# Kernel optimization log

Measured on AMD Instinct MI355X. Metric: run time of the kernel, lower is better.

Reference implementation:

```python
import jax, jax.numpy as jnp
import numpy as np

B, N, NUM_CLASSES, M, K = 64, 900, 128, 64, 8
COST_CLASS = 1.0
COST_BBOX = 5.0
INF = jnp.float32(1e9)


def _lsa(cost):
    """Jonker-Volgenant shortest-augmenting-path linear sum assignment.
    cost: [M, N] with M <= N (rows = targets, cols = predictions).
    Returns assigned column (prediction index) per row (target), shape [M] int32.
    Equivalent pairing to scipy.optimize.linear_sum_assignment."""
    Mr, Nc = cost.shape
    # column 0 is a dummy column (1-indexed columns, as in the classic formulation)
    a = jnp.concatenate([jnp.zeros((Mr, 1), cost.dtype), cost], axis=1)

    def assign_row(carry, i1):
        u, v, p = carry  # u:[M+1] row potentials, v:[N+1] col potentials, p:[N+1] row assigned to col (0=free)
        p = p.at[0].set(i1)
        init = (u, v, p,
                jnp.full(Nc + 1, INF, cost.dtype),   # minv
                jnp.zeros(Nc + 1, bool),             # used
                jnp.zeros(Nc + 1, jnp.int32),        # way (parent col)
                jnp.int32(0))                        # j0

        def cond(st):
            return st[2][st[6]] != 0

        def body(st):
            u, v, p, minv, used, way, j0 = st
            used = used.at[j0].set(True)
            i0 = p[j0]
            cur = a[i0 - 1] - u[i0] - v              # reduced costs of row i0 over all cols
            better = (cur < minv) & (~used)
            minv = jnp.where(better, cur, minv)
            way = jnp.where(better, j0, way)
            masked = jnp.where(used, INF, minv)
            j1 = jnp.argmin(masked).astype(jnp.int32)
            delta = masked[j1]
            u = u.at[p].add(jnp.where(used, delta, jnp.float32(0.0)))
            v = v - jnp.where(used, delta, jnp.float32(0.0))
            minv = jnp.where(used, minv, minv - delta)
            return (u, v, p, minv, used, way, j1)

        u, v, p, minv, used, way, j0 = jax.lax.while_loop(cond, body, init)

        def bt_body(st):  # backtrack the augmenting path
            p_, jj = st
            j1 = way[jj]
            return p_.at[jj].set(p_[j1]), j1

        p, _ = jax.lax.while_loop(lambda st: st[1] != 0, bt_body, (p, j0))
        return (u, v, p), None

    u0 = jnp.zeros(Mr + 1, cost.dtype)
    v0 = jnp.zeros(Nc + 1, cost.dtype)
    p0 = jnp.zeros(Nc + 1, jnp.int32)
    (u, v, p), _ = jax.lax.scan(assign_row, (u0, v0, p0),
                                jnp.arange(1, Mr + 1, dtype=jnp.int32))
    rows = p[1:]                                     # [N]: 1-indexed target row per pred col, 0 = free
    res = jnp.zeros(Mr, jnp.int32)
    res = res.at[jnp.where(rows > 0, rows - 1, Mr)].set(
        jnp.arange(Nc, dtype=jnp.int32), mode='drop')
    return res


def setup_inputs() -> dict:
    key = jax.random.key(0)
    k1, k2, k3, k4 = jax.random.split(key, 4)
    return {
        'class_logits': jax.random.normal(k1, (B, N, NUM_CLASSES), jnp.float32),
        'corners': jax.random.normal(k2, (B, N, K, 3), jnp.float32),
        'tgt_labels': jax.random.randint(k3, (B, M), 0, NUM_CLASSES, jnp.int32),
        'boxes': jax.random.normal(k4, (B, M, 7), jnp.float32),
    }


def reference(class_logits, corners, tgt_labels, boxes):
    probs = jax.nn.softmax(class_logits, axis=-1)                        # [B,N,C]
    idx = jnp.broadcast_to(tgt_labels[:, None, :], (B, N, M))
    class_cost = -jnp.take_along_axis(probs, idx, axis=2)               # [B,N,M]
    centers = corners.mean(axis=2)                                       # [B,N,3]
    diff = centers[:, :, None, :] - boxes[:, None, :, :3]                # [B,N,M,3]
    box_cost = jnp.sqrt(jnp.sum(diff * diff, axis=-1))                   # cdist, p=2
    C = COST_CLASS * class_cost + COST_BBOX * box_cost                   # [B,N,M]
    pred_idx = jax.vmap(_lsa)(jnp.swapaxes(C, 1, 2))                     # [B,M]: pred assigned to each target
    tgt_idx = jnp.broadcast_to(jnp.arange(M, dtype=jnp.int32), pred_idx.shape)
    return C, pred_idx, tgt_idx
```

## Files before the change

kernel.cpp:

```cpp
#include <hip/hip_runtime.h>
#include <math.h>

#define Bv   64
#define Nv   900
#define Mv   64
#define NCls 128
#define NCOLS (Nv + 1)
#define KREG 15
#define INFV 1000000000.0f
#define BIGV 1.0e18f

#define SEL15(arr, kidx, dst) do {            \
    int _s = arr[0];                          \
    _Pragma("unroll")                         \
    for (int _kk = 1; _kk < KREG; _kk++)      \
        _s = ((kidx) == _kk) ? arr[_kk] : _s; \
    (dst) = _s;                               \
} while (0)

#define SET15(arr, kidx, val) do {            \
    _Pragma("unroll")                         \
    for (int _kk = 0; _kk < KREG; _kk++)      \
        if ((kidx) == _kk) arr[_kk] = (val);  \
} while (0)

__device__ __forceinline__ float wave_min_f32(float x) {
#define MSTEP(ctrl, rmask)                                                \
    {                                                                     \
        int o = __builtin_amdgcn_update_dpp(__float_as_int(x),            \
                __float_as_int(x), ctrl, rmask, 0xf, false);              \
        x = fminf(x, __int_as_float(o));                                  \
    }
    MSTEP(0x111, 0xf) MSTEP(0x112, 0xf) MSTEP(0x114, 0xf) MSTEP(0x118, 0xf)
    MSTEP(0x142, 0xa) MSTEP(0x143, 0xc)
#undef MSTEP
    return __int_as_float(__builtin_amdgcn_readlane(__float_as_int(x), 63));
}

__device__ __forceinline__ unsigned wave_min_u32(unsigned x) {
#define USTEP(ctrl, rmask)                                                \
    {                                                                     \
        unsigned o = (unsigned)__builtin_amdgcn_update_dpp((int)x,        \
                     (int)x, ctrl, rmask, 0xf, false);                    \
        x = (o < x) ? o : x;                                              \
    }
    USTEP(0x111, 0xf) USTEP(0x112, 0xf) USTEP(0x114, 0xf) USTEP(0x118, 0xf)
    USTEP(0x142, 0xa) USTEP(0x143, 0xc)
#undef USTEP
    return (unsigned)__builtin_amdgcn_readlane((int)x, 63);
}

__device__ __forceinline__ float wave_sum_f32(float x) {
#define SSTEP(ctrl, rmask)                                                \
    {                                                                     \
        int o = __builtin_amdgcn_update_dpp(0, __float_as_int(x),         \
                                            ctrl, rmask, 0xf, false);     \
        x += __int_as_float(o);                                           \
    }
    SSTEP(0x111, 0xf) SSTEP(0x112, 0xf) SSTEP(0x114, 0xf) SSTEP(0x118, 0xf)
    SSTEP(0x142, 0xa) SSTEP(0x143, 0xc)
#undef SSTEP
    return __int_as_float(__builtin_amdgcn_readlane(__float_as_int(x), 63));
}

__global__ __launch_bounds__(256) void cost_kernel(
    const float* __restrict__ logits,
    const float* __restrict__ corners,
    const int*   __restrict__ labels,
    const float* __restrict__ boxes,
    float*       __restrict__ C)
{
    const int b = blockIdx.y;
    const int n = blockIdx.x * 4 + (threadIdx.x >> 6);
    const int t = threadIdx.x & 63;
    const long bn = (long)b * Nv + n;

    const float2 l2 = ((const float2*)(logits + bn * NCls))[t];
    const float* cp = corners + bn * 24;
    float cx = 0.f, cy = 0.f, cz = 0.f;
    if (t < 8) { cx = cp[3 * t]; cy = cp[3 * t + 1]; cz = cp[3 * t + 2]; }
    const int    lbl = labels[b * Mv + t];
    const float* bx  = boxes + ((long)b * Mv + t) * 7;
    const float bx0 = bx[0], bx1 = bx[1], bx2 = bx[2];

    float e0 = expf(l2.x), e1 = expf(l2.y);
    float s  = wave_sum_f32(e0 + e1);

    cx = wave_sum_f32(cx) * 0.125f;
    cy = wave_sum_f32(cy) * 0.125f;
    cz = wave_sum_f32(cz) * 0.125f;

    float p0 = __shfl(e0, lbl >> 1, 64);
    float p1 = __shfl(e1, lbl >> 1, 64);
    float pm = ((lbl & 1) ? p1 : p0) / s;

    float dx = cx - bx0, dy = cy - bx1, dz = cz - bx2;
    C[bn * Mv + t] = 5.0f * sqrtf(dx * dx + dy * dy + dz * dz) - pm;
}

__global__ __launch_bounds__(64) void lsa_kernel(
    const float* __restrict__ C,
    float* __restrict__ outPred, float* __restrict__ outTgt)
{
    const int b = blockIdx.x;
    const int t = threadIdx.x;
    const float* cb = C + (size_t)b * Nv * Mv;

    float mv0 = INFV, mv1 = INFV, mv2 = INFV, mv3 = INFV;
    int   mj0 = 0,    mj1 = 0,    mj2 = 0,    mj3 = 0;
    #pragma unroll 9
    for (int n = 0; n < 225; ++n) {
        float c0 = cb[(size_t)(n      ) * Mv + t];
        float c1 = cb[(size_t)(n + 225) * Mv + t];
        float c2 = cb[(size_t)(n + 450) * Mv + t];
        float c3 = cb[(size_t)(n + 675) * Mv + t];
        if (c0 < mv0) { mv0 = c0; mj0 = n;       }
        if (c1 < mv1) { mv1 = c1; mj1 = n + 225; }
        if (c2 < mv2) { mv2 = c2; mj2 = n + 450; }
        if (c3 < mv3) { mv3 = c3; mj3 = n + 675; }
    }
    float rowmin = mv0; int rown = mj0;
    if (mv1 < rowmin) { rowmin = mv1; rown = mj1; }
    if (mv2 < rowmin) { rowmin = mv2; rown = mj2; }
    if (mv3 < rowmin) { rowmin = mv3; rown = mj3; }

    float u_reg = rowmin;
    const int jcol = rown + 1;

    bool isdup = false;
    #pragma unroll
    for (int s = 1; s < 64; ++s) {
        int oj = __shfl(jcol, (t + 64 - s) & 63, 64);
        isdup |= (oj == jcol) && (s <= t);
    }
    unsigned long long pending = __ballot(isdup);

    int   p_reg[KREG], way_reg[KREG];
    float v_reg[KREG], minv[KREG], crow[KREG];
    #pragma unroll
    for (int k = 0; k < KREG; k++) { p_reg[k] = 0; way_reg[k] = 0; v_reg[k] = 0.f; }

    int rowcol = isdup ? 0 : jcol;

    #pragma unroll 8
    for (int i = 0; i < 64; ++i) {
        int jb = __shfl(jcol, i, 64);
        if (!((pending >> i) & 1ull) && t == (jb & 63))
            SET15(p_reg, jb >> 6, i + 1);
    }

    while (pending) {
        const int i1v = __ffsll(pending);
        pending &= pending - 1;

        unsigned int usedMask = (t == 0) ? 1u : 0u;
        unsigned long long rowMask = 0;
        #pragma unroll
        for (int k = 0; k < KREG; k++) minv[k] = INFV;

        int j0 = 0;
        int i0 = i1v;

        #pragma unroll
        for (int k = 0; k < KREG; k++) {
            int j = t + (k << 6);
            crow[k] = (j >= 1 && j < NCOLS)
                      ? cb[(((size_t)(j - 1)) << 6) + (i0 - 1)] : BIGV;
        }

        while (true) {
            rowMask |= 1ull << (i0 - 1);
            const int sl = __builtin_amdgcn_readfirstlane(i0 - 1);
            const float u_i0 = __int_as_float(
                __builtin_amdgcn_readlane(__float_as_int(u_reg), sl));

            float bestv = INFV;
            int   bestk = 0;
            #pragma unroll
            for (int k = 0; k < KREG; k++) {
                float cur = (crow[k] - u_i0) - v_reg[k];
                if (cur < minv[k]) { minv[k] = cur; way_reg[k] = j0; }
                if (minv[k] < bestv) { bestv = minv[k]; bestk = k; }
            }

            const float delta = wave_min_f32(bestv);

            unsigned jc = (bestv == delta)
                          ? (unsigned)(t + (bestk << 6)) : 0xFFFFFFFFu;
            const int j1 = (int)wave_min_u32(jc);

            const int k1 = j1 >> 6, l1 = j1 & 63;
            int ptmp; SEL15(p_reg, k1, ptmp);
            const int inext = __builtin_amdgcn_readlane(ptmp, l1);

            const bool newbit = (t == l1);
            unsigned newUsed = usedMask | (newbit ? (1u << k1) : 0u);
            if (inext != 0) {
                const int src = inext - 1;
                #pragma unroll
                for (int k = 0; k < KREG; k++) {
                    int j = t + (k << 6);
                    bool valid = (j >= 1 && j < NCOLS) && !((newUsed >> k) & 1u);
                    crow[k] = valid ? cb[(((size_t)(j - 1)) << 6) + src] : BIGV;
                }
            }

            if ((rowMask >> t) & 1ull) u_reg += delta;
            #pragma unroll
            for (int k = 0; k < KREG; k++) {
                bool used  = (usedMask >> k) & 1u;
                bool isnew = newbit && (k == k1);
                v_reg[k] = used ? v_reg[k] - delta : v_reg[k];
                float mupd = used ? minv[k] : minv[k] - delta;
                minv[k] = isnew ? INFV : mupd;
            }
            usedMask = newUsed;

            j0 = j1;
            i0 = inext;
            if (i0 == 0) break;
        }

        while (j0 != 0) {
            const int k0 = j0 >> 6, l0 = j0 & 63;
            int wtmp; SEL15(way_reg, k0, wtmp);
            const int jprev = __shfl(wtmp, l0, 64);
            int pv;
            if (jprev == 0) {
                pv = i1v;
            } else {
                int ptmp; SEL15(p_reg, jprev >> 6, ptmp);
                pv = __shfl(ptmp, jprev & 63, 64);
            }
            if (t == l0) SET15(p_reg, k0, pv);
            if (t == pv - 1) rowcol = j0;
            j0 = jprev;
        }
    }

    outPred[b * Mv + t] = (float)(rowcol - 1);
    outTgt[b * Mv + t]  = (float)t;
}

extern "C" void kernel_launch(void* const* d_in, const int* in_sizes, int n_in,
                              void* d_out, int out_size, void* d_ws, size_t ws_size,
                              hipStream_t stream)
{
    (void)in_sizes; (void)n_in; (void)out_size; (void)d_ws; (void)ws_size;

    const float* logits  = (const float*)d_in[0];
    const float* corners = (const float*)d_in[1];
    const int*   labels  = (const int*)  d_in[2];
    const float* boxes   = (const float*)d_in[3];

    float* out  = (float*)d_out;
    float* Cc   = out;
    float* pred = out + (size_t)Bv * Nv * Mv;
    float* tgt  = pred + (size_t)Bv * Mv;

    cost_kernel<<<dim3(225, Bv), 256, 0, stream>>>(logits, corners, labels, boxes, Cc);
    lsa_kernel<<<Bv, 64, 0, stream>>>(Cc, pred, tgt);
}
```

Measured before the change: 235.7 us.

## Defer potential updates in JV loop and fuse min/argmin wave reduction

The shortest-augmenting-path inner loop switches to cumulative distances (Dijkstra-style). Row and column potentials are updated once after each augmentation instead of subtracting delta from every register each iteration. The separate float min and index min wave reductions become one lexicographic (value, index) DPP reduction over sortable-uint encodings, and the p_reg select becomes a binary mux tree. It also prefetches the next cost row before the bookkeeping and splits the per-lane argmin into three independent chains to shorten dependency chains. The risk is floating-point differences from accumulated distances versus incremental deltas, which could change tie-breaking.

```diff
diff --git a/kernel.cpp b/kernel.cpp
--- a/kernel.cpp
+++ b/kernel.cpp
@@ -18,36 +18,59 @@
     (dst) = _s;                               \
 } while (0)
 
+#define SELTREE15(arr, kidx, dst) do {                      \
+    int _a0 = ((kidx) & 1) ? arr[1]  : arr[0];              \
+    int _a1 = ((kidx) & 1) ? arr[3]  : arr[2];              \
+    int _a2 = ((kidx) & 1) ? arr[5]  : arr[4];              \
+    int _a3 = ((kidx) & 1) ? arr[7]  : arr[6];              \
+    int _a4 = ((kidx) & 1) ? arr[9]  : arr[8];              \
+    int _a5 = ((kidx) & 1) ? arr[11] : arr[10];             \
+    int _a6 = ((kidx) & 1) ? arr[13] : arr[12];             \
+    int _a7 = arr[14];              \
+    int _b0 = ((kidx) & 2) ? _a1 : _a0;                     \
+    int _b1 = ((kidx) & 2) ? _a3 : _a2;                     \
+    int _b2 = ((kidx) & 2) ? _a5 : _a4;                     \
+    int _b3 = ((kidx) & 2) ? _a7 : _a6;                     \
+    int _c0 = ((kidx) & 4) ? _b1 : _b0;                     \
+    int _c1 = ((kidx) & 4) ? _b3 : _b2;                     \
+    (dst)   = ((kidx) & 8) ? _c1 : _c0;                     \
+} while (0)
+
 #define SET15(arr, kidx, val) do {            \
     _Pragma("unroll")                         \
     for (int _kk = 0; _kk < KREG; _kk++)      \
         if ((kidx) == _kk) arr[_kk] = (val);  \
 } while (0)
 
-__device__ __forceinline__ float wave_min_f32(float x) {
-#define MSTEP(ctrl, rmask)                                                \
-    {                                                                     \
-        int o = __builtin_amdgcn_update_dpp(__float_as_int(x),            \
-                __float_as_int(x), ctrl, rmask, 0xf, false);              \
-        x = fminf(x, __int_as_float(o));                                  \
-    }
-    MSTEP(0x111, 0xf) MSTEP(0x112, 0xf) MSTEP(0x114, 0xf) MSTEP(0x118, 0xf)
-    MSTEP(0x142, 0xa) MSTEP(0x143, 0xc)
-#undef MSTEP
-    return __int_as_float(__builtin_amdgcn_readlane(__float_as_int(x), 63));
-}
-
-__device__ __forceinline__ unsigned wave_min_u32(unsigned x) {
-#define USTEP(ctrl, rmask)                                                \
-    {                                                                     \
-        unsigned o = (unsigned)__builtin_amdgcn_update_dpp((int)x,        \
-                     (int)x, ctrl, rmask, 0xf, false);                    \
-        x = (o < x) ? o : x;                                              \
-    }
-    USTEP(0x111, 0xf) USTEP(0x112, 0xf) USTEP(0x114, 0xf) USTEP(0x118, 0xf)
-    USTEP(0x142, 0xa) USTEP(0x143, 0xc)
-#undef USTEP
-    return (unsigned)__builtin_amdgcn_readlane((int)x, 63);
+__device__ __forceinline__ unsigned f2s(float f) {
+    unsigned x = __float_as_uint(f);
+    return x ^ ((unsigned)((int)x >> 31) | 0x80000000u);
+}
+__device__ __forceinline__ float s2f(unsigned s) {
+    unsigned x = ((int)s < 0) ? (s ^ 0x80000000u) : ~s;
+    return __uint_as_float(x);
+}
+
+__device__ __forceinline__ void wave_min_pair(unsigned& hi, unsigned& lo) {
+#define DPP_STEP(ctrl, rmask)                                                   \
+    {                                                                           \
+        unsigned ohi = (unsigned)__builtin_amdgcn_update_dpp(                   \
+            (int)hi, (int)hi, ctrl, rmask, 0xf, false);                         \
+        unsigned olo = (unsigned)__builtin_amdgcn_update_dpp(                   \
+            (int)lo, (int)lo, ctrl, rmask, 0xf, false);                         \
+        bool take = (ohi < hi) || (ohi == hi && olo < lo);                      \
+        hi = take ? ohi : hi;                                                   \
+        lo = take ? olo : lo;                                                   \
+    }
+    DPP_STEP(0x111, 0xf)
+    DPP_STEP(0x112, 0xf)
+    DPP_STEP(0x114, 0xf)
+    DPP_STEP(0x118, 0xf)
+    DPP_STEP(0x142, 0xa)
+    DPP_STEP(0x143, 0xc)
+#undef DPP_STEP
+    hi = (unsigned)__builtin_amdgcn_readlane((int)hi, 63);
+    lo = (unsigned)__builtin_amdgcn_readlane((int)lo, 63);
 }
 
 __device__ __forceinline__ float wave_sum_f32(float x) {
@@ -136,7 +159,7 @@
     unsigned long long pending = __ballot(isdup);
 
     int   p_reg[KREG], way_reg[KREG];
-    float v_reg[KREG], minv[KREG], crow[KREG];
+    float v_reg[KREG], D[KREG], crow[KREG], vsel[KREG];
     #pragma unroll
     for (int k = 0; k < KREG; k++) { p_reg[k] = 0; way_reg[k] = 0; v_reg[k] = 0.f; }
 
@@ -153,72 +176,103 @@
         const int i1v = __ffsll(pending);
         pending &= pending - 1;
 
-        unsigned int usedMask = (t == 0) ? 1u : 0u;
-        unsigned long long rowMask = 0;
+        unsigned usedMask = (t == 0) ? 1u : 0u;
         #pragma unroll
-        for (int k = 0; k < KREG; k++) minv[k] = INFV;
+        for (int k = 0; k < KREG; k++) { D[k] = INFV; vsel[k] = 0.f; }
+        float uin  = (t == i1v - 1) ? 0.0f : -1.0f;
+        float dCur = 0.0f;
+        float dF   = 0.0f;
 
         int j0 = 0;
         int i0 = i1v;
 
-        #pragma unroll
-        for (int k = 0; k < KREG; k++) {
-            int j = t + (k << 6);
-            crow[k] = (j >= 1 && j < NCOLS)
-                      ? cb[(((size_t)(j - 1)) << 6) + (i0 - 1)] : BIGV;
+        {
+            const int src0 = __builtin_amdgcn_readfirstlane(i0 - 1);
+            #pragma unroll
+            for (int k = 0; k < KREG; k++) {
+                int j = t + (k << 6);
+                bool valid = (j >= 1 && j < NCOLS) && !((usedMask >> k) & 1u);
+                crow[k] = valid
+                          ? cb[(((size_t)(j - 1)) << 6) + src0] - v_reg[k] : BIGV;
+            }
         }
 
         while (true) {
-            rowMask |= 1ull << (i0 - 1);
             const int sl = __builtin_amdgcn_readfirstlane(i0 - 1);
             const float u_i0 = __int_as_float(
                 __builtin_amdgcn_readlane(__float_as_int(u_reg), sl));
-
-            float bestv = INFV;
-            int   bestk = 0;
-            #pragma unroll
-            for (int k = 0; k < KREG; k++) {
-                float cur = (crow[k] - u_i0) - v_reg[k];
-                if (cur < minv[k]) { minv[k] = cur; way_reg[k] = j0; }
-                if (minv[k] < bestv) { bestv = minv[k]; bestk = k; }
-            }
-
-            const float delta = wave_min_f32(bestv);
-
-            unsigned jc = (bestv == delta)
-                          ? (unsigned)(t + (bestk << 6)) : 0xFFFFFFFFu;
-            const int j1 = (int)wave_min_u32(jc);
+            const float h = dCur - u_i0;
+
+            float bv0 = INFV, bv1 = INFV, bv2 = INFV;
+            int   bk0 = 0,    bk1 = 5,    bk2 = 10;
+            #pragma unroll
+            for (int k = 0; k < 5; k++) {
+                float ca = crow[k] + h;
+                bool lt = ca < D[k];
+                if (lt) { D[k] = ca; way_reg[k] = j0; }
+                if (D[k] < bv0) { bv0 = D[k]; bk0 = k; }
+            }
+            #pragma unroll
+            for (int k = 5; k < 10; k++) {
+                float ca = crow[k] + h;
+                bool lt = ca < D[k];
+                if (lt) { D[k] = ca; way_reg[k] = j0; }
+                if (D[k] < bv1) { bv1 = D[k]; bk1 = k; }
+            }
+            #pragma unroll
+            for (int k = 10; k < KREG; k++) {
+                float ca = crow[k] + h;
+                bool lt = ca < D[k];
+                if (lt) { D[k] = ca; way_reg[k] = j0; }
+                if (D[k] < bv2) { bv2 = D[k]; bk2 = k; }
+            }
+            if (bv1 < bv0) { bv0 = bv1; bk0 = bk1; }
+            if (bv2 < bv0) { bv0 = bv2; bk0 = bk2; }
+
+            unsigned hi = f2s(bv0), lo = (unsigned)(t + (bk0 << 6));
+            wave_min_pair(hi, lo);
+            const float dNew = s2f(hi);
+            const int   j1   = (int)lo;
 
             const int k1 = j1 >> 6, l1 = j1 & 63;
-            int ptmp; SEL15(p_reg, k1, ptmp);
+            int ptmp; SELTREE15(p_reg, k1, ptmp);
             const int inext = __builtin_amdgcn_readlane(ptmp, l1);
 
-            const bool newbit = (t == l1);
-            unsigned newUsed = usedMask | (newbit ? (1u << k1) : 0u);
+            float pf[KREG];
             if (inext != 0) {
-                const int src = inext - 1;
+                const int src = __builtin_amdgcn_readfirstlane(inext - 1);
                 #pragma unroll
                 for (int k = 0; k < KREG; k++) {
                     int j = t + (k << 6);
-                    bool valid = (j >= 1 && j < NCOLS) && !((newUsed >> k) & 1u);
-                    crow[k] = valid ? cb[(((size_t)(j - 1)) << 6) + src] : BIGV;
+                    pf[k] = (j >= 1 && j < NCOLS)
+                            ? cb[(((size_t)(j - 1)) << 6) + src] : BIGV;
                 }
             }
 
-            if ((rowMask >> t) & 1ull) u_reg += delta;
+            const bool newbit = (t == l1);
             #pragma unroll
             for (int k = 0; k < KREG; k++) {
-                bool used  = (usedMask >> k) & 1u;
-                bool isnew = newbit && (k == k1);
-                v_reg[k] = used ? v_reg[k] - delta : v_reg[k];
-                float mupd = used ? minv[k] : minv[k] - delta;
-                minv[k] = isnew ? INFV : mupd;
-            }
-            usedMask = newUsed;
-
+                if (newbit && (k == k1)) { D[k] = BIGV; vsel[k] = dNew; }
+            }
+            usedMask |= newbit ? (1u << k1) : 0u;
+            if (t == inext - 1) uin = dNew;
+
+            dCur = dNew;
             j0 = j1;
             i0 = inext;
-            if (i0 == 0) break;
+            if (i0 == 0) { dF = dNew; break; }
+
+            #pragma unroll
+            for (int k = 0; k < KREG; k++) {
+                bool used = (usedMask >> k) & 1u;
+                crow[k] = used ? BIGV : pf[k] - v_reg[k];
+            }
+        }
+
+        if (uin >= 0.0f) u_reg += (dF - uin);
+        #pragma unroll
+        for (int k = 0; k < KREG; k++) {
+            if ((usedMask >> k) & 1u) v_reg[k] -= (dF - vsel[k]);
         }
 
         while (j0 != 0) {
@@ -229,8 +283,8 @@
             if (jprev == 0) {
                 pv = i1v;
             } else {
-                int ptmp; SEL15(p_reg, jprev >> 6, ptmp);
-                pv = __shfl(ptmp, jprev & 63, 64);
+                int ptmp2; SEL15(p_reg, jprev >> 6, ptmp2);
+                pv = __shfl(ptmp2, jprev & 63, 64);
             }
             if (t == l0) SET15(p_reg, k0, pv);
             if (t == pv - 1) rowcol = j0;
```

New measurement: 269.7 us. +14.4%, slower.
